# Kernel tuning notes

Hardware: AMD Instinct MI355X
Metric: run time of the kernel (lower is better)

## Reference

```python
import jax, jax.numpy as jnp
import numpy as np

B, C, H, W = 8, 64, 128, 128


def setup_inputs() -> dict:
    key = jax.random.key(0)
    k1, k2, k3 = jax.random.split(key, 3)
    x = jax.random.normal(k1, (B, C, H, W), dtype=jnp.float32)
    # offset conv weights: (2C, C, 3, 3), small init like the module (std=0.01)
    W_off = jax.random.normal(k2, (2 * C, C, 3, 3), dtype=jnp.float32) * 0.01
    # following regular conv: (C_out, C, 3, 3)
    W_conv = jax.random.normal(k3, (C, C, 3, 3), dtype=jnp.float32) * 0.05
    b_conv = jnp.zeros((C,), dtype=jnp.float32)
    return {"x": x, "W_off": W_off, "W_conv": W_conv, "b_conv": b_conv}


def _conv2d_same(x, w):
    return jax.lax.conv_general_dilated(
        x, w, window_strides=(1, 1), padding=[(1, 1), (1, 1)],
        dimension_numbers=("NCHW", "OIHW", "NCHW"))


def _deform_offset(x, W_off):
    """Faithful ConvOffset2D: offset conv + clamped 4-corner bilinear gather."""
    b, c, h, w = x.shape
    offsets_ = _conv2d_same(x, W_off)                    # (b, 2c, h, w)
    # torch contiguous view (b,2c,h,w) -> (b*c, h*w, 2): adjacent w elements
    # become the 2 offset components; jnp.reshape matches this exactly.
    offsets = offsets_.reshape(b * c, h * w, 2)
    xf = x.reshape(b * c, h, w)

    gy, gx = jnp.meshgrid(jnp.arange(h), jnp.arange(w), indexing="ij")
    grid = jnp.stack([gy, gx], axis=-1).reshape(-1, 2).astype(x.dtype)  # (h*w, 2)
    coords = offsets + grid[None]                        # (b*c, h*w, 2)

    cy = jnp.clip(coords[..., 0], 0.0, h - 1)
    cx = jnp.clip(coords[..., 1], 0.0, w - 1)
    y0 = jnp.floor(cy)
    y1 = jnp.ceil(cy)
    x0 = jnp.floor(cx)
    x1 = jnp.ceil(cx)

    flat = xf.reshape(-1)                                # (b*c*h*w,)
    base = (jnp.arange(b * c, dtype=jnp.int32) * (h * w))[:, None]

    def gather(yy, xx):
        idx = base + yy.astype(jnp.int32) * w + xx.astype(jnp.int32)
        return flat[idx]

    v_lt = gather(y0, x0)   # (floor y, floor x)
    v_rb = gather(y1, x1)   # (ceil y,  ceil x)
    v_lb = gather(y0, x1)   # (floor y, ceil x)
    v_rt = gather(y1, x0)   # (ceil y,  floor x)

    dy = cy - y0
    dx = cx - x0
    v_t = dy * (v_rt - v_lt) + v_lt
    v_b = dy * (v_rb - v_lb) + v_lb
    out = dx * (v_b - v_t) + v_t                         # (b*c, h*w)
    return out.reshape(b, c, h, w)


def reference(x, W_off, W_conv, b_conv):
    x_def = _deform_offset(x, W_off)
    out = _conv2d_same(x_def, W_conv) + b_conv[None, :, None, None]
    return out
```

## Files before the change

### kernel.cpp

```cpp
#include <hip/hip_runtime.h>

#define DH 128
#define DW 128
#define DB 8
#define DC 64
constexpr int HW = DH * DW;

typedef __attribute__((ext_vector_type(4))) float f32x4;
typedef __attribute__((ext_vector_type(16))) float f32x16;
typedef __attribute__((ext_vector_type(8))) short bf16x8;
typedef __attribute__((ext_vector_type(4))) unsigned int u32x4;

__device__ __forceinline__ unsigned short f2b(float f) {
    unsigned int u = __builtin_bit_cast(unsigned int, f);
    u = (u + 0x7FFFu + ((u >> 16) & 1u)) >> 16;
    return (unsigned short)u;
}
__device__ __forceinline__ float b2f(unsigned short h) {
    unsigned int u = ((unsigned int)h) << 16;
    return __builtin_bit_cast(float, u);
}

__global__ __launch_bounds__(256) void prep_kernel(
    const float* __restrict__ x, const float* __restrict__ wo,
    const float* __restrict__ wc, unsigned short* __restrict__ xh,
    unsigned short* __restrict__ wt1, unsigned short* __restrict__ wt2)
{
    __shared__ unsigned short smx[64 * 80];
    const int blk = blockIdx.x;
    const int t = threadIdx.x;
    if (blk < 2048) {
        const int b = blk >> 8;
        const int p0 = (blk & 255) * 64;
        const int ci = t >> 2, q = t & 3;
        const float* xr = x + ((size_t)b * 64 + ci) * HW + p0;
#pragma unroll
        for (int j = 0; j < 4; ++j) {
            int pix = (j * 4 + q) * 4;
            float4 v = *(const float4*)(xr + pix);
            smx[(pix + 0) * 80 + ci] = f2b(v.x);
            smx[(pix + 1) * 80 + ci] = f2b(v.y);
            smx[(pix + 2) * 80 + ci] = f2b(v.z);
            smx[(pix + 3) * 80 + ci] = f2b(v.w);
        }
        __syncthreads();
        unsigned short* outp = xh + ((size_t)b * HW + p0) * 64;
        for (int i = t; i < 512; i += 256) {
            int pix = i >> 3, cq = i & 7;
            u32x4 v = *(const u32x4*)(smx + pix * 80 + cq * 8);
            *(u32x4*)(outp + pix * 64 + cq * 8) = v;
        }
    } else {
        int id = (blk - 2048) * 256 + t;
        const int N1 = 9 * 128 * 64, N2 = 9 * 64 * 64;
        if (id < N1) {
            int tp = id / (128 * 64);
            int rem = id - tp * 128 * 64;
            int co = rem >> 6, ci = rem & 63;
            wt1[id] = f2b(wo[(co * 64 + ci) * 9 + tp]);
        } else if (id < N1 + N2) {
            int k = id - N1;
            int tp = k / (64 * 64);
            int rem = k - tp * 64 * 64;
            int co = rem >> 6, ci = rem & 63;
            wt2[k] = f2b(wc[(co * 64 + ci) * 9 + tp]);
        }
    }
}

template<int COUT, int MI, bool HWC_BF16_OUT>
__global__ __launch_bounds__(512, 4) void conv_mfma_kernel(
    const unsigned short* __restrict__ xh,
    const unsigned short* __restrict__ wt,
    const float* __restrict__ bias,
    void* __restrict__ outp)
{
    constexpr int WBYTES = COUT * 64 * 2;
    constexpr int SPASS = WBYTES / 8192;
    __shared__ char sm[41472 + 2 * WBYTES];
    char* const wbuf0 = sm + 41472;
    char* const wbuf1 = sm + 41472 + WBYTES;

    const int tid = threadIdx.x;
    const int b = blockIdx.y;
    const int ty0 = (blockIdx.x >> 3) << 4;
    const int tx0 = (blockIdx.x & 7) << 4;
    const unsigned short* xb = xh + (size_t)b * HW * 64;

    u32x4 wreg[SPASS];
    {
        const char* wsrc = (const char*)wt;
#pragma unroll
        for (int s = 0; s < SPASS; ++s) {
            int L = (s * 512 + tid) * 16;
            wreg[s] = *(const u32x4*)(wsrc + (L ^ (((L >> 7) & 7) << 4)));
        }
    }
    for (int i = tid; i < 2592; i += 512) {
        int hp = i >> 3, cq = i & 7;
        int hy = hp / 18, hx = hp - hy * 18;
        int gy = ty0 + hy - 1, gx = tx0 + hx - 1;
        u32x4 v = {0u, 0u, 0u, 0u};
        if ((unsigned)gy < 128u && (unsigned)gx < 128u)
            v = *(const u32x4*)(xb + (size_t)((gy << 7) + gx) * 64 + cq * 8);
        *(u32x4*)(sm + ((hp * 128 + cq * 16) ^ ((hp & 7) << 4))) = v;
    }
#pragma unroll
    for (int s = 0; s < SPASS; ++s) {
        int L = (s * 512 + tid) * 16;
        *(u32x4*)(wbuf0 + L) = wreg[s];
    }
    __syncthreads();

    const int lane = tid & 63;
    const int wv = tid >> 6;
    const int wm = wv & 1;
    const int wn = wv >> 1;
    const int n = lane & 31;
    const int half = lane >> 5;
    const int px = n & 15;
    const int pyb = wn * 4 + (n >> 4);
    const int swzA = (lane & 7) << 4;
    const int rowA = (wm * (MI * 32) + n) * 128 + half * 16;

    int hp0[2];
#pragma unroll
    for (int ni = 0; ni < 2; ++ni)
        hp0[ni] = (pyb + ni * 2) * 18 + px;

    f32x16 acc[MI][2];
#pragma unroll
    for (int mi = 0; mi < MI; ++mi)
#pragma unroll
        for (int ni = 0; ni < 2; ++ni)
#pragma unroll
            for (int e = 0; e < 16; ++e) acc[mi][ni][e] = 0.f;

#pragma unroll
    for (int t9 = 0; t9 < 9; ++t9) {
        const int toff = (t9 / 3) * 18 + (t9 % 3);
        const char* wb = (t9 & 1) ? wbuf1 : wbuf0;
        u32x4 wr[SPASS];
        if (t9 < 8) {
            const char* wsrc = (const char*)(wt + (size_t)(t9 + 1) * COUT * 64);
#pragma unroll
            for (int s = 0; s < SPASS; ++s) {
                int L = (s * 512 + tid) * 16;
                wr[s] = *(const u32x4*)(wsrc + (L ^ (((L >> 7) & 7) << 4)));
            }
        }
#pragma unroll
        for (int kk = 0; kk < 4; ++kk) {
            const int kcol = kk * 32;
            bf16x8 a[MI], bv[2];
#pragma unroll
            for (int mi = 0; mi < MI; ++mi)
                a[mi] = *(const bf16x8*)(wb + ((rowA + mi * 4096 + kcol) ^ swzA));
#pragma unroll
            for (int ni = 0; ni < 2; ++ni) {
                int hp = hp0[ni] + toff;
                bv[ni] = *(const bf16x8*)(sm + ((hp * 128 + kcol + half * 16) ^ ((hp & 7) << 4)));
            }
#pragma unroll
            for (int mi = 0; mi < MI; ++mi)
#pragma unroll
                for (int ni = 0; ni < 2; ++ni)
                    acc[mi][ni] = __builtin_amdgcn_mfma_f32_32x32x16_bf16(
                        a[mi], bv[ni], acc[mi][ni], 0, 0, 0);
        }
        if (t9 < 8) {
            char* wbn = ((t9 + 1) & 1) ? wbuf1 : wbuf0;
#pragma unroll
            for (int s = 0; s < SPASS; ++s) {
                int L = (s * 512 + tid) * 16;
                *(u32x4*)(wbn + L) = wr[s];
            }
        }
        __syncthreads();
    }

#pragma unroll
    for (int ni = 0; ni < 2; ++ni) {
        int py = pyb + ni * 2;
        int gp = (ty0 + py) * 128 + tx0 + px;
        if (HWC_BF16_OUT) {
            unsigned short* o = (unsigned short*)outp + ((size_t)b * HW + gp) * COUT;
#pragma unroll
            for (int mi = 0; mi < MI; ++mi) {
                int cob = wm * (MI * 32) + mi * 32 + half * 4;
#pragma unroll
                for (int g = 0; g < 4; ++g) {
                    uint2 pk;
                    pk.x = (unsigned)f2b(acc[mi][ni][g * 4 + 0]) |
                           ((unsigned)f2b(acc[mi][ni][g * 4 + 1]) << 16);
                    pk.y = (unsigned)f2b(acc[mi][ni][g * 4 + 2]) |
                           ((unsigned)f2b(acc[mi][ni][g * 4 + 3]) << 16);
                    *(uint2*)(o + cob + g * 8) = pk;
                }
            }
        } else {
            float* o = (float*)outp + (size_t)b * COUT * HW + gp;
#pragma unroll
            for (int mi = 0; mi < MI; ++mi) {
                int cob = wm * (MI * 32) + mi * 32 + half * 4;
#pragma unroll
                for (int g = 0; g < 4; ++g)
#pragma unroll
                    for (int r = 0; r < 4; ++r) {
                        int co = cob + g * 8 + r;
                        o[(size_t)co * HW] = acc[mi][ni][g * 4 + r] + bias[co];
                    }
            }
        }
    }
}

__global__ __launch_bounds__(512, 4) void conv2_deform_kernel(
    const unsigned short* __restrict__ xh,
    const unsigned short* __restrict__ offs,
    const unsigned short* __restrict__ wt,
    const float* __restrict__ bias,
    float* __restrict__ out)
{
    __shared__ char sm[41472 + 2 * 8192];
    char* const wbuf0 = sm + 41472;
    char* const wbuf1 = sm + 41472 + 8192;

    const int tid = threadIdx.x;
    const int b = blockIdx.y;
    const int ty0 = (blockIdx.x >> 3) << 4;
    const int tx0 = (blockIdx.x & 7) << 4;
    const unsigned short* xb = xh + (size_t)b * HW * 64;
    const unsigned short* ob = offs + (size_t)b * HW * 128;

    u32x4 wreg;
    {
        int L = tid * 16;
        wreg = *(const u32x4*)((const char*)wt + (L ^ (((L >> 7) & 7) << 4)));
    }

    for (int i = tid; i < 324 * 64; i += 512) {
        int hp = i >> 6, ci = i & 63;
        int hy = hp / 18, hx = hp - hy * 18;
        int gy = ty0 + hy - 1, gx = tx0 + hx - 1;
        unsigned short val = 0;
        if ((unsigned)gy < 128u && (unsigned)gx < 128u) {
            int q = (gy << 7) + gx;
            int ch = 2 * ci + (q >> 13);
            int pp = (2 * q) & (HW - 1);
            float oy = b2f(ob[(size_t)pp * 128 + ch]);
            float ox = b2f(ob[(size_t)(pp + 1) * 128 + ch]);
            float cy = fminf(fmaxf(oy + (float)gy, 0.f), 127.f);
            float cx = fminf(fmaxf(ox + (float)gx, 0.f), 127.f);
            float y0f = floorf(cy), x0f = floorf(cx);
            int y0 = (int)y0f, x0i = (int)x0f;
            int y1 = (int)ceilf(cy), x1 = (int)ceilf(cx);
            const unsigned short* pl = xb + ci;
            float v_lt = b2f(pl[(size_t)(y0 * 128 + x0i) * 64]);
            float v_rb = b2f(pl[(size_t)(y1 * 128 + x1) * 64]);
            float v_lb = b2f(pl[(size_t)(y0 * 128 + x1) * 64]);
            float v_rt = b2f(pl[(size_t)(y1 * 128 + x0i) * 64]);
            float dy = cy - y0f, dxf = cx - x0f;
            float v_t = fmaf(dy, v_rt - v_lt, v_lt);
            float v_b = fmaf(dy, v_rb - v_lb, v_lb);
            val = f2b(fmaf(dxf, v_b - v_t, v_t));
        }
        *(unsigned short*)(sm + ((hp * 128 + ci * 2) ^ ((hp & 7) << 4))) = val;
    }
    *(u32x4*)(wbuf0 + tid * 16) = wreg;
    __syncthreads();

    const int lane = tid & 63;
    const int wv = tid >> 6;
    const int wm = wv & 1;
    const int wn = wv >> 1;
    const int n = lane & 31;
    const int half = lane >> 5;
    const int px = n & 15;
    const int pyb = wn * 4 + (n >> 4);
    const int swzA = (lane & 7) << 4;
    const int rowA = (wm * 32 + n) * 128 + half * 16;

    int hp0[2];
#pragma unroll
    for (int ni = 0; ni < 2; ++ni)
        hp0[ni] = (pyb + ni * 2) * 18 + px;

    f32x16 acc[2];
#pragma unroll
    for (int ni = 0; ni < 2; ++ni)
#pragma unroll
        for (int e = 0; e < 16; ++e) acc[ni][e] = 0.f;

#pragma unroll
    for (int t9 = 0; t9 < 9; ++t9) {
        const int toff = (t9 / 3) * 18 + (t9 % 3);
        const char* wb = (t9 & 1) ? wbuf1 : wbuf0;
        u32x4 wr;
        if (t9 < 8) {
            const char* wsrc = (const char*)(wt + (size_t)(t9 + 1) * 64 * 64);
            int L = tid * 16;
            wr = *(const u32x4*)(wsrc + (L ^ (((L >> 7) & 7) << 4)));
        }
#pragma unroll
        for (int kk = 0; kk < 4; ++kk) {
            const int kcol = kk * 32;
            bf16x8 a = *(const bf16x8*)(wb + ((rowA + kcol) ^ swzA));
            bf16x8 bv[2];
#pragma unroll
            for (int ni = 0; ni < 2; ++ni) {
                int hp = hp0[ni] + toff;
                bv[ni] = *(const bf16x8*)(sm + ((hp * 128 + kcol + half * 16) ^ ((hp & 7) << 4)));
            }
#pragma unroll
            for (int ni = 0; ni < 2; ++ni)
                acc[ni] = __builtin_amdgcn_mfma_f32_32x32x16_bf16(
                    a, bv[ni], acc[ni], 0, 0, 0);
        }
        if (t9 < 8) {
            char* wbn = ((t9 + 1) & 1) ? wbuf1 : wbuf0;
            *(u32x4*)(wbn + tid * 16) = wr;
        }
        __syncthreads();
    }

#pragma unroll
    for (int ni = 0; ni < 2; ++ni) {
        int py = pyb + ni * 2;
        int gp = (ty0 + py) * 128 + tx0 + px;
        float* o = out + (size_t)b * 64 * HW + gp;
        int cob = wm * 32 + half * 4;
#pragma unroll
        for (int g = 0; g < 4; ++g)
#pragma unroll
            for (int r = 0; r < 4; ++r) {
                int co = cob + g * 8 + r;
                o[(size_t)co * HW] = acc[ni][g * 4 + r] + bias[co];
            }
    }
}

extern "C" void kernel_launch(void* const* d_in, const int* in_sizes, int n_in,
                              void* d_out, int out_size, void* d_ws, size_t ws_size,
                              hipStream_t stream) {
    const float* x      = (const float*)d_in[0];
    const float* W_off  = (const float*)d_in[1];
    const float* W_conv = (const float*)d_in[2];
    const float* b_conv = (const float*)d_in[3];

    unsigned short* xh   = (unsigned short*)d_ws;
    unsigned short* offs = xh + (size_t)DB * HW * 64;
    unsigned short* wt1  = offs + (size_t)DB * HW * 128;
    unsigned short* wt2  = wt1 + 9 * 128 * 64;
    float* out = (float*)d_out;

    prep_kernel<<<2048 + 432, 256, 0, stream>>>(x, W_off, W_conv, xh, wt1, wt2);

    conv_mfma_kernel<128, 2, true><<<dim3(64, DB), 512, 0, stream>>>(
        xh, wt1, nullptr, offs);

    conv2_deform_kernel<<<dim3(64, DB), 512, 0, stream>>>(
        xh, offs, wt2, b_conv, out);
}
```

Before: 163.3 us.

## Read conv weights directly from global memory and store offsets channel-major

Both conv kernels stop staging weights through double-buffered LDS and instead load MFMA A fragments straight from global memory (cached in L1/L2), which removes the per-tap __syncthreads and shrinks LDS use. The offset conv now writes its bf16 output in NCHW (channel-major) layout rather than HWC. The deform gather then reads both offset components as one 32-bit load from contiguous memory. The deform loop is also unrolled explicitly. The trade-off is more global load latency on the weight fragments inside the MFMA loop, plus strided per-channel stores in conv1.

```diff
diff --git a/kernel.cpp b/kernel.cpp
--- a/kernel.cpp
+++ b/kernel.cpp
@@ -68,34 +68,18 @@
     }
 }
 
-template<int COUT, int MI, bool HWC_BF16_OUT>
-__global__ __launch_bounds__(512, 4) void conv_mfma_kernel(
+__global__ __launch_bounds__(512, 4) void conv1_kernel(
     const unsigned short* __restrict__ xh,
     const unsigned short* __restrict__ wt,
-    const float* __restrict__ bias,
-    void* __restrict__ outp)
+    unsigned short* __restrict__ outp)
 {
-    constexpr int WBYTES = COUT * 64 * 2;
-    constexpr int SPASS = WBYTES / 8192;
-    __shared__ char sm[41472 + 2 * WBYTES];
-    char* const wbuf0 = sm + 41472;
-    char* const wbuf1 = sm + 41472 + WBYTES;
-
+    __shared__ char sm[41472];
     const int tid = threadIdx.x;
     const int b = blockIdx.y;
     const int ty0 = (blockIdx.x >> 3) << 4;
     const int tx0 = (blockIdx.x & 7) << 4;
     const unsigned short* xb = xh + (size_t)b * HW * 64;
 
-    u32x4 wreg[SPASS];
-    {
-        const char* wsrc = (const char*)wt;
-#pragma unroll
-        for (int s = 0; s < SPASS; ++s) {
-            int L = (s * 512 + tid) * 16;
-            wreg[s] = *(const u32x4*)(wsrc + (L ^ (((L >> 7) & 7) << 4)));
-        }
-    }
     for (int i = tid; i < 2592; i += 512) {
         int hp = i >> 3, cq = i & 7;
         int hy = hp / 18, hx = hp - hy * 18;
@@ -103,12 +87,8 @@
         u32x4 v = {0u, 0u, 0u, 0u};
         if ((unsigned)gy < 128u && (unsigned)gx < 128u)
             v = *(const u32x4*)(xb + (size_t)((gy << 7) + gx) * 64 + cq * 8);
+        *(u32x4*)(sm + ((hp * 128 + cq * 16) ^ ((hp & 7) << 4)));
         *(u32x4*)(sm + ((hp * 128 + cq * 16) ^ ((hp & 7) << 4))) = v;
-    }
-#pragma unroll
-    for (int s = 0; s < SPASS; ++s) {
-        int L = (s * 512 + tid) * 16;
-        *(u32x4*)(wbuf0 + L) = wreg[s];
     }
     __syncthreads();
 
@@ -120,17 +100,16 @@
     const int half = lane >> 5;
     const int px = n & 15;
     const int pyb = wn * 4 + (n >> 4);
-    const int swzA = (lane & 7) << 4;
-    const int rowA = (wm * (MI * 32) + n) * 128 + half * 16;
+    const int cobase = wm * 64;
 
     int hp0[2];
 #pragma unroll
     for (int ni = 0; ni < 2; ++ni)
         hp0[ni] = (pyb + ni * 2) * 18 + px;
 
-    f32x16 acc[MI][2];
-#pragma unroll
-    for (int mi = 0; mi < MI; ++mi)
+    f32x16 acc[2][2];
+#pragma unroll
+    for (int mi = 0; mi < 2; ++mi)
 #pragma unroll
         for (int ni = 0; ni < 2; ++ni)
 #pragma unroll
@@ -139,78 +118,39 @@
 #pragma unroll
     for (int t9 = 0; t9 < 9; ++t9) {
         const int toff = (t9 / 3) * 18 + (t9 % 3);
-        const char* wb = (t9 & 1) ? wbuf1 : wbuf0;
-        u32x4 wr[SPASS];
-        if (t9 < 8) {
-            const char* wsrc = (const char*)(wt + (size_t)(t9 + 1) * COUT * 64);
-#pragma unroll
-            for (int s = 0; s < SPASS; ++s) {
-                int L = (s * 512 + tid) * 16;
-                wr[s] = *(const u32x4*)(wsrc + (L ^ (((L >> 7) & 7) << 4)));
-            }
-        }
 #pragma unroll
         for (int kk = 0; kk < 4; ++kk) {
-            const int kcol = kk * 32;
-            bf16x8 a[MI], bv[2];
-#pragma unroll
-            for (int mi = 0; mi < MI; ++mi)
-                a[mi] = *(const bf16x8*)(wb + ((rowA + mi * 4096 + kcol) ^ swzA));
+            bf16x8 a[2], bv[2];
+#pragma unroll
+            for (int mi = 0; mi < 2; ++mi)
+                a[mi] = *(const bf16x8*)(wt +
+                    (size_t)(t9 * 128 + cobase + mi * 32 + n) * 64 + kk * 16 + half * 8);
 #pragma unroll
             for (int ni = 0; ni < 2; ++ni) {
                 int hp = hp0[ni] + toff;
-                bv[ni] = *(const bf16x8*)(sm + ((hp * 128 + kcol + half * 16) ^ ((hp & 7) << 4)));
+                bv[ni] = *(const bf16x8*)(sm + ((hp * 128 + kk * 32 + half * 16) ^ ((hp & 7) << 4)));
             }
 #pragma unroll
-            for (int mi = 0; mi < MI; ++mi)
+            for (int mi = 0; mi < 2; ++mi)
 #pragma unroll
                 for (int ni = 0; ni < 2; ++ni)
                     acc[mi][ni] = __builtin_amdgcn_mfma_f32_32x32x16_bf16(
                         a[mi], bv[ni], acc[mi][ni], 0, 0, 0);
         }
-        if (t9 < 8) {
-            char* wbn = ((t9 + 1) & 1) ? wbuf1 : wbuf0;
-#pragma unroll
-            for (int s = 0; s < SPASS; ++s) {
-                int L = (s * 512 + tid) * 16;
-                *(u32x4*)(wbn + L) = wr[s];
-            }
-        }
-        __syncthreads();
-    }
-
+    }
+
+    unsigned short* ob = outp + (size_t)b * 128 * HW;
 #pragma unroll
     for (int ni = 0; ni < 2; ++ni) {
-        int py = pyb + ni * 2;
-        int gp = (ty0 + py) * 128 + tx0 + px;
-        if (HWC_BF16_OUT) {
-            unsigned short* o = (unsigned short*)outp + ((size_t)b * HW + gp) * COUT;
-#pragma unroll
-            for (int mi = 0; mi < MI; ++mi) {
-                int cob = wm * (MI * 32) + mi * 32 + half * 4;
-#pragma unroll
-                for (int g = 0; g < 4; ++g) {
-                    uint2 pk;
-                    pk.x = (unsigned)f2b(acc[mi][ni][g * 4 + 0]) |
-                           ((unsigned)f2b(acc[mi][ni][g * 4 + 1]) << 16);
-                    pk.y = (unsigned)f2b(acc[mi][ni][g * 4 + 2]) |
-                           ((unsigned)f2b(acc[mi][ni][g * 4 + 3]) << 16);
-                    *(uint2*)(o + cob + g * 8) = pk;
-                }
-            }
-        } else {
-            float* o = (float*)outp + (size_t)b * COUT * HW + gp;
-#pragma unroll
-            for (int mi = 0; mi < MI; ++mi) {
-                int cob = wm * (MI * 32) + mi * 32 + half * 4;
-#pragma unroll
-                for (int g = 0; g < 4; ++g)
-#pragma unroll
-                    for (int r = 0; r < 4; ++r) {
-                        int co = cob + g * 8 + r;
-                        o[(size_t)co * HW] = acc[mi][ni][g * 4 + r] + bias[co];
-                    }
-            }
+        int gp = (ty0 + pyb + ni * 2) * 128 + tx0 + px;
+#pragma unroll
+        for (int mi = 0; mi < 2; ++mi) {
+            int cob = cobase + mi * 32 + half * 4;
+#pragma unroll
+            for (int g = 0; g < 4; ++g)
+#pragma unroll
+                for (int r = 0; r < 4; ++r)
+                    ob[(size_t)(cob + g * 8 + r) * HW + gp] = f2b(acc[mi][ni][g * 4 + r]);
         }
     }
 }
@@ -222,24 +162,15 @@
     const float* __restrict__ bias,
     float* __restrict__ out)
 {
-    __shared__ char sm[41472 + 2 * 8192];
-    char* const wbuf0 = sm + 41472;
-    char* const wbuf1 = sm + 41472 + 8192;
-
+    __shared__ char sm[41472];
     const int tid = threadIdx.x;
     const int b = blockIdx.y;
     const int ty0 = (blockIdx.x >> 3) << 4;
     const int tx0 = (blockIdx.x & 7) << 4;
     const unsigned short* xb = xh + (size_t)b * HW * 64;
-    const unsigned short* ob = offs + (size_t)b * HW * 128;
-
-    u32x4 wreg;
-    {
-        int L = tid * 16;
-        wreg = *(const u32x4*)((const char*)wt + (L ^ (((L >> 7) & 7) << 4)));
-    }
-
-    for (int i = tid; i < 324 * 64; i += 512) {
+    const unsigned short* ob = offs + (size_t)b * 128 * HW;
+
+    auto deform_one = [&](int i) {
         int hp = i >> 6, ci = i & 63;
         int hy = hp / 18, hx = hp - hy * 18;
         int gy = ty0 + hy - 1, gx = tx0 + hx - 1;
@@ -247,9 +178,10 @@
         if ((unsigned)gy < 128u && (unsigned)gx < 128u) {
             int q = (gy << 7) + gx;
             int ch = 2 * ci + (q >> 13);
-            int pp = (2 * q) & (HW - 1);
-            float oy = b2f(ob[(size_t)pp * 128 + ch]);
-            float ox = b2f(ob[(size_t)(pp + 1) * 128 + ch]);
+            int u = q & 8191;
+            unsigned o2 = *(const unsigned*)(ob + (size_t)ch * HW + 2 * u);
+            float oy = b2f((unsigned short)(o2 & 0xffffu));
+            float ox = b2f((unsigned short)(o2 >> 16));
             float cy = fminf(fmaxf(oy + (float)gy, 0.f), 127.f);
             float cx = fminf(fmaxf(ox + (float)gx, 0.f), 127.f);
             float y0f = floorf(cy), x0f = floorf(cx);
@@ -266,8 +198,10 @@
             val = f2b(fmaf(dxf, v_b - v_t, v_t));
         }
         *(unsigned short*)(sm + ((hp * 128 + ci * 2) ^ ((hp & 7) << 4))) = val;
-    }
-    *(u32x4*)(wbuf0 + tid * 16) = wreg;
+    };
+#pragma unroll 4
+    for (int k = 0; k < 40; ++k) deform_one(tid + k * 512);
+    if (tid < 256) deform_one(tid + 40 * 512);
     __syncthreads();
 
     const int lane = tid & 63;
@@ -278,8 +212,7 @@
     const int half = lane >> 5;
     const int px = n & 15;
     const int pyb = wn * 4 + (n >> 4);
-    const int swzA = (lane & 7) << 4;
-    const int rowA = (wm * 32 + n) * 128 + half * 16;
+    const int cobase = wm * 32;
 
     int hp0[2];
 #pragma unroll
@@ -295,41 +228,28 @@
 #pragma unroll
     for (int t9 = 0; t9 < 9; ++t9) {
         const int toff = (t9 / 3) * 18 + (t9 % 3);
-        const char* wb = (t9 & 1) ? wbuf1 : wbuf0;
-        u32x4 wr;
-        if (t9 < 8) {
-            const char* wsrc = (const char*)(wt + (size_t)(t9 + 1) * 64 * 64);
-            int L = tid * 16;
-            wr = *(const u32x4*)(wsrc + (L ^ (((L >> 7) & 7) << 4)));
-        }
 #pragma unroll
         for (int kk = 0; kk < 4; ++kk) {
-            const int kcol = kk * 32;
-            bf16x8 a = *(const bf16x8*)(wb + ((rowA + kcol) ^ swzA));
+            bf16x8 a = *(const bf16x8*)(wt +
+                (size_t)(t9 * 64 + cobase + n) * 64 + kk * 16 + half * 8);
             bf16x8 bv[2];
 #pragma unroll
             for (int ni = 0; ni < 2; ++ni) {
                 int hp = hp0[ni] + toff;
-                bv[ni] = *(const bf16x8*)(sm + ((hp * 128 + kcol + half * 16) ^ ((hp & 7) << 4)));
+                bv[ni] = *(const bf16x8*)(sm + ((hp * 128 + kk * 32 + half * 16) ^ ((hp & 7) << 4)));
             }
 #pragma unroll
             for (int ni = 0; ni < 2; ++ni)
                 acc[ni] = __builtin_amdgcn_mfma_f32_32x32x16_bf16(
                     a, bv[ni], acc[ni], 0, 0, 0);
         }
-        if (t9 < 8) {
-            char* wbn = ((t9 + 1) & 1) ? wbuf1 : wbuf0;
-            *(u32x4*)(wbn + tid * 16) = wr;
-        }
-        __syncthreads();
     }
 
 #pragma unroll
     for (int ni = 0; ni < 2; ++ni) {
-        int py = pyb + ni * 2;
-        int gp = (ty0 + py) * 128 + tx0 + px;
+        int gp = (ty0 + pyb + ni * 2) * 128 + tx0 + px;
         float* o = out + (size_t)b * 64 * HW + gp;
-        int cob = wm * 32 + half * 4;
+        int cob = cobase + half * 4;
 #pragma unroll
         for (int g = 0; g < 4; ++g)
 #pragma unroll
@@ -356,8 +276,7 @@
 
     prep_kernel<<<2048 + 432, 256, 0, stream>>>(x, W_off, W_conv, xh, wt1, wt2);
 
-    conv_mfma_kernel<128, 2, true><<<dim3(64, DB), 512, 0, stream>>>(
-        xh, wt1, nullptr, offs);
+    conv1_kernel<<<dim3(64, DB), 512, 0, stream>>>(xh, wt1, offs);
 
     conv2_deform_kernel<<<dim3(64, DB), 512, 0, stream>>>(
         xh, offs, wt2, b_conv, out);
```

New measurement: 222.2 us. 1.36x slower.
